# Kernel optimization log

Hardware: AMD Instinct MI355X
Metric: run time of the kernel (lower is better)

## Reference

```python
import jax, jax.numpy as jnp
import numpy as np

B, LQ, LA = 128, 128, 512
VOCAB, EMB, FILT, K = 50000, 300, 400, 3
EPS = 1e-8


def setup_inputs() -> dict:
    key = jax.random.key(0)
    kq, ka, ke, kw, kb, kW = jax.random.split(key, 6)
    questions = jax.random.randint(kq, (B, LQ), 0, VOCAB + 1, dtype=jnp.int32)
    answers = jax.random.randint(ka, (B, LA), 0, VOCAB + 1, dtype=jnp.int32)
    emb = jax.random.normal(ke, (VOCAB + 1, EMB), dtype=jnp.float32) * 0.1
    emb = emb.at[0].set(0.0)  # padding_idx=0
    fan_in = EMB * K
    bound = 1.0 / np.sqrt(fan_in)
    conv_w = jax.random.uniform(kw, (FILT, EMB, K), jnp.float32, -bound, bound)
    conv_b = jax.random.uniform(kb, (FILT,), jnp.float32, -bound, bound)
    W = jax.random.normal(kW, (FILT, FILT), dtype=jnp.float32)  # init.normal_(std=1)
    return {"questions": questions, "answers": answers, "emb": emb,
            "conv_w": conv_w, "conv_b": conv_b, "W": W}


def _encode(tokens, emb, conv_w, conv_b):
    # tokens [B,L] -> embed [B,L,E] -> transpose to NCH [B,E,L] -> conv1d pad=1
    x = emb[tokens].transpose(0, 2, 1)
    y = jax.lax.conv_general_dilated(
        x, conv_w, window_strides=(1,), padding=[(1, 1)],
        dimension_numbers=("NCH", "OIH", "NCH"))
    return y + conv_b[None, :, None]  # [B, FILT, L]


def reference(questions, answers, emb, conv_w, conv_b, W):
    Q = _encode(questions, emb, conv_w, conv_b)  # [B,F,Lq]
    A = _encode(answers, emb, conv_w, conv_b)    # [B,F,La]
    # G = tanh(Q^T W A)  -> [B, Lq, La]
    G = jnp.tanh(jnp.einsum("bfq,fg,bga->bqa", Q, W, A))
    roQ = jax.nn.softmax(jnp.max(G, axis=2), axis=1)  # [B,Lq]
    roA = jax.nn.softmax(jnp.max(G, axis=1), axis=1)  # [B,La]
    rQ = jnp.einsum("bfq,bq->bf", Q, roQ)  # [B,F]
    rA = jnp.einsum("bfa,ba->bf", A, roA)  # [B,F]
    nQ = jnp.maximum(jnp.linalg.norm(rQ, axis=1), EPS)
    nA = jnp.maximum(jnp.linalg.norm(rA, axis=1), EPS)
    return jnp.sum(rQ * rA, axis=1) / (nQ * nA)  # [B]
```

## Files before the change

kernel.cpp:

```cpp
#include <hip/hip_runtime.h>
#include <hip/hip_bf16.h>

#define BB   128
#define LQ   128
#define LA   512
#define EMBD 300
#define FILT 400
#define KW   3

#define NT   25
#define KC   30
#define KCF  13
#define MT   32

typedef unsigned short u16;
typedef unsigned int   u32;
typedef __attribute__((ext_vector_type(4))) int    i32x4;
typedef __attribute__((ext_vector_type(4))) float  f32x4;
typedef __attribute__((ext_vector_type(8))) __bf16 bf16x8;

__device__ __forceinline__ u16 f2b(float f){
  u32 u = __float_as_uint(f);
  u32 r = (u + 0x7FFFu + ((u >> 16) & 1u)) >> 16;
  return (u16)r;
}
__device__ __forceinline__ u32 encf(float f){
  u32 u = __float_as_uint(f);
  return (u & 0x80000000u) ? ~u : (u | 0x80000000u);
}
__device__ __forceinline__ float decf(u32 k){
  u32 u = (k & 0x80000000u) ? (k ^ 0x80000000u) : ~k;
  return __uint_as_float(u);
}
__device__ __forceinline__ bf16x8 bzero(){
  i32x4 z; z.x = 0; z.y = 0; z.z = 0; z.w = 0;
  return __builtin_bit_cast(bf16x8, z);
}

__global__ void k_prep(const float* __restrict__ cw, const float* __restrict__ W,
                       u32* __restrict__ wTf, u32* __restrict__ wF){
  int idx = blockIdx.x * 256 + threadIdx.x;
  const int N1 = KC * NT * 64;
  const int N2 = KCF * NT * 64;
  if (idx < N1){
    int kc  = idx / (NT * 64);
    int rem = idx - kc * (NT * 64);
    int nt  = rem >> 6;
    int lane = rem & 63;
    int n = nt * 16 + (lane & 15);
    int quad = lane >> 4;
    u32 pack[4];
    #pragma unroll
    for (int d = 0; d < 4; d++){
      u16 h[2];
      #pragma unroll
      for (int s = 0; s < 2; s++){
        int kp = kc * 32 + quad * 8 + 2 * d + s;
        int kk = kp / 320, e = kp - kk * 320;
        float v = (e < EMBD) ? cw[(size_t)n * (EMBD * KW) + e * KW + kk] : 0.f;
        h[s] = f2b(v);
      }
      pack[d] = (u32)h[0] | ((u32)h[1] << 16);
    }
    i32x4 o; o.x = pack[0]; o.y = pack[1]; o.z = pack[2]; o.w = pack[3];
    *((i32x4*)wTf + idx) = o;
  } else if (idx < N1 + N2){
    int id2 = idx - N1;
    int kc  = id2 / (NT * 64);
    int rem = id2 - kc * (NT * 64);
    int nt  = rem >> 6;
    int lane = rem & 63;
    int n = nt * 16 + (lane & 15);
    int quad = lane >> 4;
    u32 pack[4];
    #pragma unroll
    for (int d = 0; d < 4; d++){
      u16 h[2];
      #pragma unroll
      for (int s = 0; s < 2; s++){
        int k = kc * 32 + quad * 8 + 2 * d + s;
        float v = (k < FILT) ? W[(size_t)k * FILT + n] : 0.f;
        h[s] = f2b(v);
      }
      pack[d] = (u32)h[0] | ((u32)h[1] << 16);
    }
    i32x4 o; o.x = pack[0]; o.y = pack[1]; o.z = pack[2]; o.w = pack[3];
    *((i32x4*)wF + id2) = o;
  }
}

__global__ __launch_bounds__(256) void k_encode_mfma(const int* __restrict__ toks,
    const float* __restrict__ emb, const u32* __restrict__ wTf,
    const float* __restrict__ bias, u16* __restrict__ out, int L){
  __shared__ u16 At[34 * 328];

  const int tid  = threadIdx.x;
  const int w    = tid >> 6;
  const int lane = tid & 63;
  const int col  = lane & 15;
  const int quad = lane >> 4;
  const int half = blockIdx.y;
  const int base_nt = half ? 13 : 0;
  const bool has4 = (half == 0) && (w == 0);
  const int row0 = blockIdx.x * MT;
  const int b    = row0 / L;
  const int l0   = row0 - b * L;

  int tk[10], cc[10], rws[10];
  #pragma unroll
  for (int u = 0; u < 10; u++){
    int idx = tid + 256 * u;
    tk[u] = -1; cc[u] = 0; rws[u] = 0;
    if (idx < 34 * 75){
      int r = idx / 75, c4 = idx - r * 75;
      int pos = l0 - 1 + r;
      cc[u] = c4;
      rws[u] = (r * 328 + c4 * 4) >> 1;
      if ((unsigned)pos < (unsigned)L) tk[u] = toks[b * L + pos];
    }
  }
  for (int i = tid; i < 34 * 328 / 2; i += 256) ((u32*)At)[i] = 0u;
  __syncthreads();
  {
    const float4* emb4 = (const float4*)emb;
    float4 v[10];
    #pragma unroll
    for (int u = 0; u < 10; u++)
      if (tk[u] >= 0) v[u] = emb4[(size_t)tk[u] * 75 + cc[u]];
    #pragma unroll
    for (int u = 0; u < 10; u++){
      if (tk[u] >= 0){
        u32 p0 = (u32)f2b(v[u].x) | ((u32)f2b(v[u].y) << 16);
        u32 p1 = (u32)f2b(v[u].z) | ((u32)f2b(v[u].w) << 16);
        ((u32*)At)[rws[u]]     = p0;
        ((u32*)At)[rws[u] + 1] = p1;
      }
    }
  }

  f32x4 acc[4][2];
  #pragma unroll
  for (int j = 0; j < 4; j++)
    #pragma unroll
    for (int mf = 0; mf < 2; mf++)
      acc[j][mf] = (f32x4){0.f, 0.f, 0.f, 0.f};

  __syncthreads();

  const i32x4* bbase = (const i32x4*)wTf + (size_t)(base_nt + w) * 64 + lane;
  i32x4 Bb[2][4];
  i32x4 Ab[2][2];
  {
    #pragma unroll
    for (int j = 0; j < 3; j++) Bb[0][j] = bbase[(4 * j) * 64];
    if (has4) Bb[0][3] = bbase[12 * 64];
    const int ebase0 = quad * 8;
    Ab[0][0] = *(const i32x4*)(At + (col) * 328 + ebase0);
    Ab[0][1] = *(const i32x4*)(At + (16 + col) * 328 + ebase0);
  }
  #pragma unroll
  for (int kc = 0; kc < KC; kc++){
    const int cur = kc & 1;
    if (kc + 1 < KC){
      const i32x4* s = bbase + (size_t)(kc + 1) * (NT * 64);
      #pragma unroll
      for (int j = 0; j < 3; j++) Bb[cur ^ 1][j] = s[(4 * j) * 64];
      if (has4) Bb[cur ^ 1][3] = s[12 * 64];
      const int kk1 = (kc + 1) / 10, e01 = ((kc + 1) - kk1 * 10) * 32;
      const int ebase1 = e01 + quad * 8;
      Ab[cur ^ 1][0] = *(const i32x4*)(At + (col + kk1) * 328 + ebase1);
      Ab[cur ^ 1][1] = *(const i32x4*)(At + (16 + col + kk1) * 328 + ebase1);
    }
    bf16x8 a0 = __builtin_bit_cast(bf16x8, Ab[cur][0]);
    bf16x8 a1 = __builtin_bit_cast(bf16x8, Ab[cur][1]);
    #pragma unroll
    for (int j = 0; j < 3; j++){
      bf16x8 bf = __builtin_bit_cast(bf16x8, Bb[cur][j]);
      acc[j][0] = __builtin_amdgcn_mfma_f32_16x16x32_bf16(a0, bf, acc[j][0], 0, 0, 0);
      acc[j][1] = __builtin_amdgcn_mfma_f32_16x16x32_bf16(a1, bf, acc[j][1], 0, 0, 0);
    }
    if (has4){
      bf16x8 bf = __builtin_bit_cast(bf16x8, Bb[cur][3]);
      acc[3][0] = __builtin_amdgcn_mfma_f32_16x16x32_bf16(a0, bf, acc[3][0], 0, 0, 0);
      acc[3][1] = __builtin_amdgcn_mfma_f32_16x16x32_bf16(a1, bf, acc[3][1], 0, 0, 0);
    }
  }

  #pragma unroll
  for (int j = 0; j < 4; j++){
    if (j == 3 && !has4) continue;
    int n = (base_nt + w + 4 * j) * 16 + col;
    float bv = bias[n];
    #pragma unroll
    for (int mf = 0; mf < 2; mf++){
      int rbase = row0 + mf * 16 + quad * 4;
      #pragma unroll
      for (int r = 0; r < 4; r++)
        out[(size_t)(rbase + r) * FILT + n] = f2b(acc[j][mf][r] + bv);
    }
  }
}

__global__ __launch_bounds__(512) void k_mid(const u16* __restrict__ QT,
    const u32* __restrict__ wF, const u16* __restrict__ AT,
    u32* __restrict__ rme, u32* __restrict__ cme){
  __shared__ u16 Ts[64 * 408];
  __shared__ float cpart[256][5];
  const int tid  = threadIdx.x;
  const int w    = tid >> 6;
  const int lane = tid & 63;
  const int col  = lane & 15;
  const int quad = lane >> 4;
  const int z    = blockIdx.x;
  const int qh   = blockIdx.y;
  const int b    = blockIdx.z;
  const int wq   = w & 3;
  const int wh   = w >> 2;

  {
    const int bnt = wh ? 13 : 0;
    const int cnt = wh ? 12 : 13;
    const u16* arow = QT + (size_t)(b * LQ + qh * 64 + wq * 16 + col) * FILT;
    const i32x4* wFp = (const i32x4*)wF;
    for (int ntc = 0; ntc < 3; ntc++){
      const int nleft = cnt - ntc * 5;
      f32x4 acc[5];
      #pragma unroll
      for (int j = 0; j < 5; j++) acc[j] = (f32x4){0.f, 0.f, 0.f, 0.f};
      i32x4 Ab[2], Bb[2][5];
      Ab[0] = *(const i32x4*)(arow + quad * 8);
      #pragma unroll
      for (int j = 0; j < 5; j++)
        if (j < nleft) Bb[0][j] = wFp[(size_t)(bnt + ntc * 5 + j) * 64 + lane];
      for (int kc = 0; kc < KCF; kc++){
        const int cur = kc & 1;
        if (kc + 1 < KCF){
          Ab[cur ^ 1] = *(const i32x4*)(arow + (kc + 1) * 32 + quad * 8);
          #pragma unroll
          for (int j = 0; j < 5; j++)
            if (j < nleft)
              Bb[cur ^ 1][j] = wFp[((size_t)(kc + 1) * NT + bnt + ntc * 5 + j) * 64 + lane];
        }
        bf16x8 a = __builtin_bit_cast(bf16x8, Ab[cur]);
        #pragma unroll
        for (int j = 0; j < 5; j++)
          if (j < nleft)
            acc[j] = __builtin_amdgcn_mfma_f32_16x16x32_bf16(a,
                       __builtin_bit_cast(bf16x8, Bb[cur][j]), acc[j], 0, 0, 0);
      }
      #pragma unroll
      for (int j = 0; j < 5; j++){
        if (j < nleft){
          int g = (bnt + ntc * 5 + j) * 16 + col;
          #pragma unroll
          for (int r = 0; r < 4; r++)
            Ts[(wq * 16 + quad * 4 + r) * 408 + g] = f2b(acc[j][r]);
        }
      }
    }
  }
  __syncthreads();

  float rm[4];
  #pragma unroll
  for (int r = 0; r < 4; r++) rm[r] = -3.4e38f;
  const u16* Tsrow = Ts + (wq * 16 + col) * 408;
  for (int atg = 0; atg < 2; atg++){
    f32x4 acc[4];
    #pragma unroll
    for (int i = 0; i < 4; i++) acc[i] = (f32x4){0.f, 0.f, 0.f, 0.f};
    const u16* ar[4];
    #pragma unroll
    for (int i = 0; i < 4; i++)
      ar[i] = AT + (size_t)(b * LA + z * 256 + (wh * 8 + atg * 4 + i) * 16 + col) * FILT;
    i32x4 Ab2[2], Bb2[2][4];
    Ab2[0] = *(const i32x4*)(Tsrow + quad * 8);
    #pragma unroll
    for (int i = 0; i < 4; i++) Bb2[0][i] = *(const i32x4*)(ar[i] + quad * 8);
    for (int kc = 0; kc < KCF; kc++){
      const int cur = kc & 1;
      if (kc + 1 < KCF){
        int off = (kc + 1) * 32 + quad * 8;
        Ab2[cur ^ 1] = *(const i32x4*)(Tsrow + off);
        #pragma unroll
        for (int i = 0; i < 4; i++) Bb2[cur ^ 1][i] = *(const i32x4*)(ar[i] + off);
      }
      const bool live = (kc < 12) || (quad < 2);
      bf16x8 a = live ? __builtin_bit_cast(bf16x8, Ab2[cur]) : bzero();
      #pragma unroll
      for (int i = 0; i < 4; i++)
        acc[i] = __builtin_amdgcn_mfma_f32_16x16x32_bf16(a,
                   __builtin_bit_cast(bf16x8, Bb2[cur][i]), acc[i], 0, 0, 0);
    }
    #pragma unroll
    for (int i = 0; i < 4; i++){
      float cmx = fmaxf(fmaxf(acc[i][0], acc[i][1]), fmaxf(acc[i][2], acc[i][3]));
      cmx = fmaxf(cmx, __shfl_xor(cmx, 16));
      cmx = fmaxf(cmx, __shfl_xor(cmx, 32));
      if (quad == 0) cpart[(wh * 8 + atg * 4 + i) * 16 + col][wq] = cmx;
      #pragma unroll
      for (int r = 0; r < 4; r++) rm[r] = fmaxf(rm[r], acc[i][r]);
    }
  }
  #pragma unroll
  for (int r = 0; r < 4; r++){
    float m = rm[r];
    m = fmaxf(m, __shfl_xor(m, 1));
    m = fmaxf(m, __shfl_xor(m, 2));
    m = fmaxf(m, __shfl_xor(m, 4));
    m = fmaxf(m, __shfl_xor(m, 8));
    if (col == 0)
      atomicMax(&rme[b * LQ + qh * 64 + wq * 16 + quad * 4 + r], encf(m));
  }
  __syncthreads();
  if (tid < 256){
    float m = cpart[tid][0];
    #pragma unroll
    for (int s = 1; s < 4; s++) m = fmaxf(m, cpart[tid][s]);
    atomicMax(&cme[b * LA + z * 256 + tid], encf(m));
  }
}

__global__ __launch_bounds__(512) void k_tail(const u16* __restrict__ QT,
    const u16* __restrict__ AT, const u32* __restrict__ rme,
    const u32* __restrict__ cme, float* __restrict__ outp){
  __shared__ float roq[128];
  __shared__ float roa[512];
  __shared__ float red[4];
  __shared__ float rqp[8][400];
  __shared__ float rap[8][400];
  __shared__ float fin[8][3];
  const int tid = threadIdx.x, w = tid >> 6, lane = tid & 63;
  const int b = blockIdx.x;
  if (tid < 128) roq[tid] = tanhf(decf(rme[b * LQ + tid]));
  roa[tid] = tanhf(decf(cme[b * LA + tid]));
  __syncthreads();
  if (w == 0){
    float m = fmaxf(roq[lane], roq[lane + 64]);
    #pragma unroll
    for (int off = 32; off; off >>= 1) m = fmaxf(m, __shfl_down(m, off));
    if (lane == 0) red[0] = m;
  } else if (w == 1){
    float m = roa[lane];
    #pragma unroll
    for (int i = 1; i < 8; i++) m = fmaxf(m, roa[lane + 64 * i]);
    #pragma unroll
    for (int off = 32; off; off >>= 1) m = fmaxf(m, __shfl_down(m, off));
    if (lane == 0) red[1] = m;
  }
  __syncthreads();
  if (tid < 128) roq[tid] = __expf(roq[tid] - red[0]);
  roa[tid] = __expf(roa[tid] - red[1]);
  __syncthreads();
  if (w == 0){
    float s = roq[lane] + roq[lane + 64];
    #pragma unroll
    for (int off = 32; off; off >>= 1) s += __shfl_down(s, off);
    if (lane == 0) red[2] = s;
  } else if (w == 1){
    float s = 0.f;
    #pragma unroll
    for (int i = 0; i < 8; i++) s += roa[lane + 64 * i];
    #pragma unroll
    for (int off = 32; off; off >>= 1) s += __shfl_down(s, off);
    if (lane == 0) red[3] = s;
  }
  __syncthreads();
  if (tid < 128) roq[tid] *= (1.f / red[2]);
  roa[tid] *= (1.f / red[3]);
  __syncthreads();
  {
    const u32* qp = (const u32*)(QT + (size_t)(b * LQ + w * 16) * FILT);
    const u32* ap = (const u32*)(AT + (size_t)(b * LA + w * 64) * FILT);
    #pragma unroll
    for (int i = 0; i < 4; i++){
      int g = lane + 64 * i;
      if (g < FILT / 2){
        float rq0 = 0.f, rq1 = 0.f, ra0 = 0.f, ra1 = 0.f;
        for (int q = 0; q < 16; q++){
          u32 u = qp[q * (FILT / 2) + g];
          float wv = roq[w * 16 + q];
          rq0 += __uint_as_float(u << 16) * wv;
          rq1 += __uint_as_float(u & 0xFFFF0000u) * wv;
        }
        for (int a = 0; a < 64; a++){
          u32 u = ap[a * (FILT / 2) + g];
          float wv = roa[w * 64 + a];
          ra0 += __uint_as_float(u << 16) * wv;
          ra1 += __uint_as_float(u & 0xFFFF0000u) * wv;
        }
        rqp[w][2 * g] = rq0; rqp[w][2 * g + 1] = rq1;
        rap[w][2 * g] = ra0; rap[w][2 * g + 1] = ra1;
      }
    }
  }
  __syncthreads();
  float d = 0.f, n1 = 0.f, n2 = 0.f;
  if (tid < FILT){
    float rq = 0.f, ra = 0.f;
    #pragma unroll
    for (int s = 0; s < 8; s++){ rq += rqp[s][tid]; ra += rap[s][tid]; }
    d = rq * ra; n1 = rq * rq; n2 = ra * ra;
  }
  #pragma unroll
  for (int off = 32; off; off >>= 1){
    d  += __shfl_down(d, off);
    n1 += __shfl_down(n1, off);
    n2 += __shfl_down(n2, off);
  }
  if (lane == 0){ fin[w][0] = d; fin[w][1] = n1; fin[w][2] = n2; }
  __syncthreads();
  if (tid == 0){
    float D = 0.f, N1 = 0.f, N2 = 0.f;
    #pragma unroll
    for (int s = 0; s < 8; s++){ D += fin[s][0]; N1 += fin[s][1]; N2 += fin[s][2]; }
    outp[b] = D / (fmaxf(sqrtf(N1), 1e-8f) * fmaxf(sqrtf(N2), 1e-8f));
  }
}

extern "C" void kernel_launch(void* const* d_in, const int* in_sizes, int n_in,
                              void* d_out, int out_size, void* d_ws, size_t ws_size,
                              hipStream_t stream){
  const int*   qtok = (const int*)d_in[0];
  const int*   atok = (const int*)d_in[1];
  const float* emb  = (const float*)d_in[2];
  const float* cw   = (const float*)d_in[3];
  const float* cb   = (const float*)d_in[4];
  const float* W    = (const float*)d_in[5];
  float* outp = (float*)d_out;

  char* ws = (char*)d_ws;
  size_t off = 0;
  auto alloc = [&](size_t bytes) -> char* {
    char* p = ws + off;
    off = (off + bytes + 255) & ~(size_t)255;
    return p;
  };
  u32*   wTf = (u32*)alloc((size_t)KC * NT * 64 * 16);
  u32*   wF  = (u32*)alloc((size_t)KCF * NT * 64 * 16);
  u16*   QT  = (u16*)alloc((size_t)BB * LQ * FILT * 2);
  u16*   AT  = (u16*)alloc((size_t)BB * LA * FILT * 2);
  u32*   rme = (u32*)alloc((size_t)BB * LQ * 4);
  u32*   cme = (u32*)alloc((size_t)BB * LA * 4);

  hipMemsetAsync(rme, 0, (size_t)BB * LQ * 4 + (size_t)BB * LA * 4, stream);

  const int NPREP = KC * NT * 64 + KCF * NT * 64;
  k_prep<<<dim3((NPREP + 255) / 256), 256, 0, stream>>>(cw, W, wTf, wF);
  k_encode_mfma<<<dim3(BB * LQ / MT, 2), 256, 0, stream>>>(qtok, emb, wTf, cb, QT, LQ);
  k_encode_mfma<<<dim3(BB * LA / MT, 2), 256, 0, stream>>>(atok, emb, wTf, cb, AT, LA);
  k_mid<<<dim3(2, 2, BB), 512, 0, stream>>>(QT, wF, AT, rme, cme);
  k_tail<<<dim3(BB), 512, 0, stream>>>(QT, AT, rme, cme, outp);
}
```

Baseline: 276.2 us.

## Merge Q/A encode launches, widen mid-kernel tile, split tail into pool and cosine

Merges the two encode launches into one grid whose blocks pick the question or answer path by index, cutting a launch and filling the GPU better. The mid kernel drops its two-pass loop and computes all 8 answer tiles in one pass with 8 accumulators, which raises register pressure. The tail kernel is split into a pooling kernel spread over 4 slices per batch and a small cosine kernel. This adds a workspace round trip and one more launch in exchange for more parallelism.

```diff
diff --git a/kernel.cpp b/kernel.cpp
--- a/kernel.cpp
+++ b/kernel.cpp
@@ -89,9 +89,10 @@
   }
 }
 
-__global__ __launch_bounds__(256) void k_encode_mfma(const int* __restrict__ toks,
-    const float* __restrict__ emb, const u32* __restrict__ wTf,
-    const float* __restrict__ bias, u16* __restrict__ out, int L){
+__global__ __launch_bounds__(256) void k_encode_all(const int* __restrict__ qtok,
+    const int* __restrict__ atok, const float* __restrict__ emb,
+    const u32* __restrict__ wTf, const float* __restrict__ bias,
+    u16* __restrict__ outQ, u16* __restrict__ outA){
   __shared__ u16 At[34 * 328];
 
   const int tid  = threadIdx.x;
@@ -102,7 +103,13 @@
   const int half = blockIdx.y;
   const int base_nt = half ? 13 : 0;
   const bool has4 = (half == 0) && (w == 0);
-  const int row0 = blockIdx.x * MT;
+  const int nA = BB * LA / MT;
+  const bool isA = ((int)blockIdx.x < nA);
+  const int bi = isA ? blockIdx.x : (blockIdx.x - nA);
+  const int L  = isA ? LA : LQ;
+  const int* toks = isA ? atok : qtok;
+  u16* out = isA ? outA : outQ;
+  const int row0 = bi * MT;
   const int b    = row0 / L;
   const int l0   = row0 - b * L;
 
@@ -265,39 +272,38 @@
   #pragma unroll
   for (int r = 0; r < 4; r++) rm[r] = -3.4e38f;
   const u16* Tsrow = Ts + (wq * 16 + col) * 408;
-  for (int atg = 0; atg < 2; atg++){
-    f32x4 acc[4];
-    #pragma unroll
-    for (int i = 0; i < 4; i++) acc[i] = (f32x4){0.f, 0.f, 0.f, 0.f};
-    const u16* ar[4];
-    #pragma unroll
-    for (int i = 0; i < 4; i++)
-      ar[i] = AT + (size_t)(b * LA + z * 256 + (wh * 8 + atg * 4 + i) * 16 + col) * FILT;
-    i32x4 Ab2[2], Bb2[2][4];
+  {
+    f32x4 acc[8];
+    #pragma unroll
+    for (int i = 0; i < 8; i++) acc[i] = (f32x4){0.f, 0.f, 0.f, 0.f};
+    const u16* ar = AT + (size_t)(b * LA + z * 256 + wh * 128 + col) * FILT;
+    i32x4 Ab2[2], Bb2[2][8];
     Ab2[0] = *(const i32x4*)(Tsrow + quad * 8);
     #pragma unroll
-    for (int i = 0; i < 4; i++) Bb2[0][i] = *(const i32x4*)(ar[i] + quad * 8);
+    for (int i = 0; i < 8; i++)
+      Bb2[0][i] = *(const i32x4*)(ar + (size_t)(i * 16) * FILT + quad * 8);
     for (int kc = 0; kc < KCF; kc++){
       const int cur = kc & 1;
       if (kc + 1 < KCF){
         int off = (kc + 1) * 32 + quad * 8;
         Ab2[cur ^ 1] = *(const i32x4*)(Tsrow + off);
         #pragma unroll
-        for (int i = 0; i < 4; i++) Bb2[cur ^ 1][i] = *(const i32x4*)(ar[i] + off);
+        for (int i = 0; i < 8; i++)
+          Bb2[cur ^ 1][i] = *(const i32x4*)(ar + (size_t)(i * 16) * FILT + off);
       }
       const bool live = (kc < 12) || (quad < 2);
       bf16x8 a = live ? __builtin_bit_cast(bf16x8, Ab2[cur]) : bzero();
       #pragma unroll
-      for (int i = 0; i < 4; i++)
+      for (int i = 0; i < 8; i++)
         acc[i] = __builtin_amdgcn_mfma_f32_16x16x32_bf16(a,
                    __builtin_bit_cast(bf16x8, Bb2[cur][i]), acc[i], 0, 0, 0);
     }
     #pragma unroll
-    for (int i = 0; i < 4; i++){
+    for (int i = 0; i < 8; i++){
       float cmx = fmaxf(fmaxf(acc[i][0], acc[i][1]), fmaxf(acc[i][2], acc[i][3]));
       cmx = fmaxf(cmx, __shfl_xor(cmx, 16));
       cmx = fmaxf(cmx, __shfl_xor(cmx, 32));
-      if (quad == 0) cpart[(wh * 8 + atg * 4 + i) * 16 + col][wq] = cmx;
+      if (quad == 0) cpart[(wh * 8 + i) * 16 + col][wq] = cmx;
       #pragma unroll
       for (int r = 0; r < 4; r++) rm[r] = fmaxf(rm[r], acc[i][r]);
     }
@@ -321,86 +327,88 @@
   }
 }
 
-__global__ __launch_bounds__(512) void k_tail(const u16* __restrict__ QT,
+__global__ __launch_bounds__(256) void k_pool(const u16* __restrict__ QT,
     const u16* __restrict__ AT, const u32* __restrict__ rme,
-    const u32* __restrict__ cme, float* __restrict__ outp){
-  __shared__ float roq[128];
-  __shared__ float roa[512];
+    const u32* __restrict__ cme, float* __restrict__ rqp, float* __restrict__ rap){
+  __shared__ float sq[128];
+  __shared__ float sa[512];
   __shared__ float red[4];
-  __shared__ float rqp[8][400];
-  __shared__ float rap[8][400];
-  __shared__ float fin[8][3];
-  const int tid = threadIdx.x, w = tid >> 6, lane = tid & 63;
-  const int b = blockIdx.x;
-  if (tid < 128) roq[tid] = tanhf(decf(rme[b * LQ + tid]));
-  roa[tid] = tanhf(decf(cme[b * LA + tid]));
-  __syncthreads();
-  if (w == 0){
-    float m = fmaxf(roq[lane], roq[lane + 64]);
+  const int s = blockIdx.x, b = blockIdx.y, tid = threadIdx.x;
+  if (tid < 128) sq[tid] = tanhf(decf(rme[b * LQ + tid]));
+  sa[tid]       = tanhf(decf(cme[b * LA + tid]));
+  sa[tid + 256] = tanhf(decf(cme[b * LA + 256 + tid]));
+  __syncthreads();
+  if (tid < 64){
+    float m = fmaxf(sq[tid], sq[tid + 64]);
     #pragma unroll
     for (int off = 32; off; off >>= 1) m = fmaxf(m, __shfl_down(m, off));
-    if (lane == 0) red[0] = m;
-  } else if (w == 1){
-    float m = roa[lane];
-    #pragma unroll
-    for (int i = 1; i < 8; i++) m = fmaxf(m, roa[lane + 64 * i]);
+    if (tid == 0) red[0] = m;
+  } else if (tid < 128){
+    int l = tid - 64;
+    float m = sa[l];
+    #pragma unroll
+    for (int i = 1; i < 8; i++) m = fmaxf(m, sa[l + 64 * i]);
     #pragma unroll
     for (int off = 32; off; off >>= 1) m = fmaxf(m, __shfl_down(m, off));
-    if (lane == 0) red[1] = m;
-  }
-  __syncthreads();
-  if (tid < 128) roq[tid] = __expf(roq[tid] - red[0]);
-  roa[tid] = __expf(roa[tid] - red[1]);
-  __syncthreads();
-  if (w == 0){
-    float s = roq[lane] + roq[lane + 64];
-    #pragma unroll
-    for (int off = 32; off; off >>= 1) s += __shfl_down(s, off);
-    if (lane == 0) red[2] = s;
-  } else if (w == 1){
-    float s = 0.f;
-    #pragma unroll
-    for (int i = 0; i < 8; i++) s += roa[lane + 64 * i];
-    #pragma unroll
-    for (int off = 32; off; off >>= 1) s += __shfl_down(s, off);
-    if (lane == 0) red[3] = s;
-  }
-  __syncthreads();
-  if (tid < 128) roq[tid] *= (1.f / red[2]);
-  roa[tid] *= (1.f / red[3]);
-  __syncthreads();
-  {
-    const u32* qp = (const u32*)(QT + (size_t)(b * LQ + w * 16) * FILT);
-    const u32* ap = (const u32*)(AT + (size_t)(b * LA + w * 64) * FILT);
-    #pragma unroll
-    for (int i = 0; i < 4; i++){
-      int g = lane + 64 * i;
-      if (g < FILT / 2){
-        float rq0 = 0.f, rq1 = 0.f, ra0 = 0.f, ra1 = 0.f;
-        for (int q = 0; q < 16; q++){
-          u32 u = qp[q * (FILT / 2) + g];
-          float wv = roq[w * 16 + q];
-          rq0 += __uint_as_float(u << 16) * wv;
-          rq1 += __uint_as_float(u & 0xFFFF0000u) * wv;
-        }
-        for (int a = 0; a < 64; a++){
-          u32 u = ap[a * (FILT / 2) + g];
-          float wv = roa[w * 64 + a];
-          ra0 += __uint_as_float(u << 16) * wv;
-          ra1 += __uint_as_float(u & 0xFFFF0000u) * wv;
-        }
-        rqp[w][2 * g] = rq0; rqp[w][2 * g + 1] = rq1;
-        rap[w][2 * g] = ra0; rap[w][2 * g + 1] = ra1;
-      }
-    }
-  }
-  __syncthreads();
+    if (l == 0) red[1] = m;
+  }
+  __syncthreads();
+  if (tid < 128) sq[tid] = __expf(sq[tid] - red[0]);
+  sa[tid]       = __expf(sa[tid] - red[1]);
+  sa[tid + 256] = __expf(sa[tid + 256] - red[1]);
+  __syncthreads();
+  if (tid < 64){
+    float v = sq[tid] + sq[tid + 64];
+    #pragma unroll
+    for (int off = 32; off; off >>= 1) v += __shfl_down(v, off);
+    if (tid == 0) red[2] = v;
+  } else if (tid < 128){
+    int l = tid - 64;
+    float v = 0.f;
+    #pragma unroll
+    for (int i = 0; i < 8; i++) v += sa[l + 64 * i];
+    #pragma unroll
+    for (int off = 32; off; off >>= 1) v += __shfl_down(v, off);
+    if (l == 0) red[3] = v;
+  }
+  __syncthreads();
+  if (tid < 128) sq[tid] *= (1.f / red[2]);
+  sa[tid]       *= (1.f / red[3]);
+  sa[tid + 256] *= (1.f / red[3]);
+  __syncthreads();
+  if (tid < FILT / 2){
+    const u32* qp = (const u32*)(QT + (size_t)(b * LQ + s * 32) * FILT) + tid;
+    const u32* ap = (const u32*)(AT + (size_t)(b * LA + s * 128) * FILT) + tid;
+    float rq0 = 0.f, rq1 = 0.f, ra0 = 0.f, ra1 = 0.f;
+    for (int q = 0; q < 32; q++){
+      u32 u = qp[q * (FILT / 2)];
+      float wv = sq[s * 32 + q];
+      rq0 += __uint_as_float(u << 16) * wv;
+      rq1 += __uint_as_float(u & 0xFFFF0000u) * wv;
+    }
+    for (int a = 0; a < 128; a++){
+      u32 u = ap[a * (FILT / 2)];
+      float wv = sa[s * 128 + a];
+      ra0 += __uint_as_float(u << 16) * wv;
+      ra1 += __uint_as_float(u & 0xFFFF0000u) * wv;
+    }
+    size_t base = ((size_t)b * 4 + s) * FILT + 2 * tid;
+    rqp[base] = rq0; rqp[base + 1] = rq1;
+    rap[base] = ra0; rap[base + 1] = ra1;
+  }
+}
+
+__global__ __launch_bounds__(256) void k_cos(const float* __restrict__ rqp,
+    const float* __restrict__ rap, float* __restrict__ outp){
+  __shared__ float rd[4], r1[4], r2[4];
+  int b = blockIdx.x, tid = threadIdx.x;
+  int lane = tid & 63, w = tid >> 6;
   float d = 0.f, n1 = 0.f, n2 = 0.f;
-  if (tid < FILT){
-    float rq = 0.f, ra = 0.f;
-    #pragma unroll
-    for (int s = 0; s < 8; s++){ rq += rqp[s][tid]; ra += rap[s][tid]; }
-    d = rq * ra; n1 = rq * rq; n2 = ra * ra;
+  for (int f = tid; f < FILT; f += 256){
+    size_t base = (size_t)b * 4 * FILT + f;
+    float rq = rqp[base] + rqp[base + FILT] + rqp[base + 2 * FILT] + rqp[base + 3 * FILT];
+    float ra = rap[base] + rap[base + FILT] + rap[base + 2 * FILT] + rap[base + 3 * FILT];
+    d += rq * ra; n1 += rq * rq; n2 += ra * ra;
   }
   #pragma unroll
   for (int off = 32; off; off >>= 1){
@@ -408,12 +416,12 @@
     n1 += __shfl_down(n1, off);
     n2 += __shfl_down(n2, off);
   }
-  if (lane == 0){ fin[w][0] = d; fin[w][1] = n1; fin[w][2] = n2; }
+  if (lane == 0){ rd[w] = d; r1[w] = n1; r2[w] = n2; }
   __syncthreads();
   if (tid == 0){
-    float D = 0.f, N1 = 0.f, N2 = 0.f;
-    #pragma unroll
-    for (int s = 0; s < 8; s++){ D += fin[s][0]; N1 += fin[s][1]; N2 += fin[s][2]; }
+    float D  = rd[0] + rd[1] + rd[2] + rd[3];
+    float N1 = r1[0] + r1[1] + r1[2] + r1[3];
+    float N2 = r2[0] + r2[1] + r2[2] + r2[3];
     outp[b] = D / (fmaxf(sqrtf(N1), 1e-8f) * fmaxf(sqrtf(N2), 1e-8f));
   }
 }
@@ -442,13 +450,17 @@
   u16*   AT  = (u16*)alloc((size_t)BB * LA * FILT * 2);
   u32*   rme = (u32*)alloc((size_t)BB * LQ * 4);
   u32*   cme = (u32*)alloc((size_t)BB * LA * 4);
+  float* rqp = (float*)alloc((size_t)BB * 4 * FILT * 4);
+  float* rap = (float*)alloc((size_t)BB * 4 * FILT * 4);
 
   hipMemsetAsync(rme, 0, (size_t)BB * LQ * 4 + (size_t)BB * LA * 4, stream);
 
   const int NPREP = KC * NT * 64 + KCF * NT * 64;
+  const int nA = BB * LA / MT;
+  const int nQ = BB * LQ / MT;
   k_prep<<<dim3((NPREP + 255) / 256), 256, 0, stream>>>(cw, W, wTf, wF);
-  k_encode_mfma<<<dim3(BB * LQ / MT, 2), 256, 0, stream>>>(qtok, emb, wTf, cb, QT, LQ);
-  k_encode_mfma<<<dim3(BB * LA / MT, 2), 256, 0, stream>>>(atok, emb, wTf, cb, AT, LA);
+  k_encode_all<<<dim3(nA + nQ, 2), 256, 0, stream>>>(qtok, atok, emb, wTf, cb, QT, AT);
   k_mid<<<dim3(2, 2, BB), 512, 0, stream>>>(QT, wF, AT, rme, cme);
-  k_tail<<<dim3(BB), 512, 0, stream>>>(QT, AT, rme, cme, outp);
-}
+  k_pool<<<dim3(4, BB), 256, 0, stream>>>(QT, AT, rme, cme, rqp, rap);
+  k_cos<<<dim3(BB), 256, 0, stream>>>(rqp, rap, outp);
+}
```

New measurement: 270.6 us. 1.02x faster.
